# Performance work log

Hardware: AMD Instinct MI355X
Metric: run time of the kernel (lower is better)

The kernel has to match this reference:

```python
import jax, jax.numpy as jnp
import numpy as np

B, S, D, SIZE = 32, 2048, 1024, 1024

def setup_inputs() -> dict:
    key = jax.random.key(0)
    k1, k2, k3, k4, k5 = jax.random.split(key, 5)
    return {
        "inputs": jax.random.normal(k1, (B, S, D), dtype=jnp.float32),
        "g": jax.random.normal(k2, (B, D), dtype=jnp.float32),
        "WO": jax.random.normal(k3, (SIZE, D), dtype=jnp.float32) * 0.05,
        "WG": jax.random.normal(k4, (SIZE, D), dtype=jnp.float32) * 0.05,
        "v": jax.random.normal(k5, (1, SIZE), dtype=jnp.float32) * 0.05,
    }

def reference(inputs, g, WO, WG, v):
    # term1[b,s,k] = WO @ inputs[b,s]; term2[b,k] = WG @ g[b]
    term1 = jnp.einsum('kd,bsd->bsk', WO, inputs)
    term2 = jnp.einsum('kd,bd->bk', WG, g)
    tan_sum = jnp.tanh(term1 + term2[:, None, :])  # [B,S,SIZE]
    # final[b,s] = v @ tan_sum[b,s]  (v is [1,SIZE]); squeeze -> [B,S]
    return jnp.einsum('k,bsk->bs', v[0], tan_sum)
```

## Files before the change

### kernel.cpp

```cpp
#include <hip/hip_runtime.h>
#include <hip/hip_bf16.h>

#define BB   32
#define SS   2048
#define DD   1024
#define SZ   1024
#define MM   (BB*SS)

typedef short bf16x8 __attribute__((ext_vector_type(8)));
typedef float f32x4  __attribute__((ext_vector_type(4)));

__device__ __forceinline__ unsigned short f2bf(float x) {
    unsigned u = __float_as_uint(x);
    u += 0x7fffu + ((u >> 16) & 1u);
    return (unsigned short)(u >> 16);
}
__device__ __forceinline__ unsigned pack2_bf16(float a, float b) {
    return (unsigned)f2bf(a) | ((unsigned)f2bf(b) << 16);
}

__device__ __forceinline__ float ftanh(float x) {
    float e = __expf(2.0f * x);
    return 1.0f - 2.0f / (e + 1.0f);
}

__global__ void prep_kernel(const float* __restrict__ WO,
                            const float* __restrict__ WG,
                            const float* __restrict__ g,
                            unsigned short* __restrict__ WOb,
                            float* __restrict__ term2) {
    int bid = blockIdx.x, tid = threadIdx.x;
    if (bid < 1024) {
        int q = bid;
        int d = tid * 4;
        float4 w = *(const float4*)(WO + (size_t)q * DD + d);
        unsigned p0 = pack2_bf16(w.x, w.y), p1 = pack2_bf16(w.z, w.w);
        int dst = ((d >> 5) * 4096 + ((d >> 3) & 3) * 1024 + q) * 8 + (d & 7);
        *(uint2*)&WOb[dst] = make_uint2(p0, p1);
    } else {
        int id    = bid - 1024;
        int b     = id >> 4;
        int wave  = tid >> 6, lane = tid & 63;
        int kbase = (id & 15) * 64 + wave * 16;
        const float* gr = g + (size_t)b * DD + lane * 16;
        float4 g0 = *(const float4*)(gr + 0);
        float4 g1 = *(const float4*)(gr + 4);
        float4 g2 = *(const float4*)(gr + 8);
        float4 g3 = *(const float4*)(gr + 12);
        #pragma unroll
        for (int i = 0; i < 16; i++) {
            int k = kbase + i;
            const float* wr = WG + (size_t)k * DD + lane * 16;
            float4 a0 = *(const float4*)(wr + 0);
            float4 a1 = *(const float4*)(wr + 4);
            float4 a2 = *(const float4*)(wr + 8);
            float4 a3 = *(const float4*)(wr + 12);
            float s = a0.x*g0.x + a0.y*g0.y + a0.z*g0.z + a0.w*g0.w
                    + a1.x*g1.x + a1.y*g1.y + a1.z*g1.z + a1.w*g1.w
                    + a2.x*g2.x + a2.y*g2.y + a2.z*g2.z + a2.w*g2.w
                    + a3.x*g3.x + a3.y*g3.y + a3.z*g3.z + a3.w*g3.w;
            #pragma unroll
            for (int m = 1; m < 64; m <<= 1) s += __shfl_xor(s, m);
            if (lane == 0) term2[b * SZ + k] = s;
        }
    }
}

__global__ __launch_bounds__(256, 2) void fused_main(
    const float* __restrict__ Ain,
    const unsigned short* __restrict__ WOb,
    const float* __restrict__ term2,
    const float* __restrict__ v,
    float* __restrict__ out) {
    __shared__ unsigned short Abuf[2][4096];
    __shared__ unsigned short Bbuf[2][8192];
    __shared__ float part[2][128];

    const int tid  = threadIdx.x;
    const int wave = tid >> 6;
    const int lane = tid & 63;
    const int wm  = wave & 1, wn = wave >> 1;
    const int l15 = lane & 15;
    const int k8  = lane >> 4;

    const int bid     = blockIdx.x;
    const int logical = (bid & 7) * 256 + (bid >> 3);
    const int ntile = logical & 3;
    const int mtile = logical >> 2;
    const int m0 = mtile * 128;
    const int n0 = ntile * 256;
    const int bidx = m0 >> 11;

    f32x4 acc[4][8];
    #pragma unroll
    for (int i = 0; i < 4; i++)
        #pragma unroll
        for (int j = 0; j < 8; j++) acc[i][j] = (f32x4){0.f, 0.f, 0.f, 0.f};

    float4 areg[4];

    auto LOAD_A = [&](int k0) {
        #pragma unroll
        for (int r = 0; r < 4; r++) {
            int row = r * 32 + (tid >> 3);
            areg[r] = *(const float4*)(Ain + (size_t)(m0 + row) * DD + k0 + (tid & 7) * 4);
        }
    };
    auto WRITE_A = [&](int buf) {
        const int q = tid & 7, kg = q >> 1, half = q & 1;
        #pragma unroll
        for (int r = 0; r < 4; r++) {
            int row = r * 32 + (tid >> 3);
            unsigned p0 = pack2_bf16(areg[r].x, areg[r].y);
            unsigned p1 = pack2_bf16(areg[r].z, areg[r].w);
            *(uint2*)&Abuf[buf][(kg * 128 + row) * 8 + half * 4] = make_uint2(p0, p1);
        }
    };
    auto STAGE_B = [&](int buf, int kt) {
        #pragma unroll
        for (int r = 0; r < 4; r++) {
            const unsigned short* src = WOb + ((size_t)(kt * 4 + r) * 1024 + n0 + tid) * 8;
            __builtin_amdgcn_global_load_lds(
                (const __attribute__((address_space(1))) void*)src,
                (__attribute__((address_space(3))) void*)(&Bbuf[buf][(r * 256 + tid) * 8]),
                16, 0, 0);
        }
    };
    auto COMPUTE = [&](int buf) {
        bf16x8 afr[4], bfr[8];
        const int aoff = (k8 * 128 + wm * 64 + l15) * 8;
        const int boff = (k8 * 256 + wn * 128 + l15) * 8;
        #pragma unroll
        for (int mi = 0; mi < 4; mi++)
            afr[mi] = *(const bf16x8*)&Abuf[buf][aoff + mi * 128];
        #pragma unroll
        for (int ni = 0; ni < 8; ni++)
            bfr[ni] = *(const bf16x8*)&Bbuf[buf][boff + ni * 128];
        __builtin_amdgcn_s_setprio(1);
        #pragma unroll
        for (int ni = 0; ni < 8; ni++)
            #pragma unroll
            for (int mi = 0; mi < 4; mi++)
                acc[mi][ni] = __builtin_amdgcn_mfma_f32_16x16x32_bf16(
                    afr[mi], bfr[ni], acc[mi][ni], 0, 0, 0);
        __builtin_amdgcn_s_setprio(0);
    };

    LOAD_A(0);
    WRITE_A(0);
    __builtin_amdgcn_sched_barrier(0);
    STAGE_B(0, 0);
    __builtin_amdgcn_sched_barrier(0);
    LOAD_A(32);
    __builtin_amdgcn_sched_barrier(0);
    asm volatile("s_waitcnt vmcnt(4)" ::: "memory");
    asm volatile("s_waitcnt lgkmcnt(0)" ::: "memory");
    __builtin_amdgcn_sched_barrier(0);
    __builtin_amdgcn_s_barrier();

    for (int t = 0; t < 31; ++t) {
        const int buf = t & 1;
        WRITE_A(buf ^ 1);
        __builtin_amdgcn_sched_barrier(0);
        STAGE_B(buf ^ 1, t + 1);
        __builtin_amdgcn_sched_barrier(0);
        LOAD_A(((t + 2 <= 31) ? t + 2 : 31) << 5);
        __builtin_amdgcn_sched_barrier(0);
        COMPUTE(buf);
        __builtin_amdgcn_sched_barrier(0);
        asm volatile("s_waitcnt vmcnt(4)" ::: "memory");
        asm volatile("s_waitcnt lgkmcnt(0)" ::: "memory");
        __builtin_amdgcn_sched_barrier(0);
        __builtin_amdgcn_s_barrier();
    }
    COMPUTE(1);

    float rsum[4][4];
    #pragma unroll
    for (int mi = 0; mi < 4; mi++)
        #pragma unroll
        for (int r = 0; r < 4; r++) rsum[mi][r] = 0.f;

    #pragma unroll
    for (int ni = 0; ni < 8; ni++) {
        int gn = n0 + wn * 128 + ni * 16 + l15;
        float t2 = term2[bidx * SZ + gn];
        float vv = v[gn];
        #pragma unroll
        for (int mi = 0; mi < 4; mi++)
            #pragma unroll
            for (int r = 0; r < 4; r++)
                rsum[mi][r] += ftanh(acc[mi][ni][r] + t2) * vv;
    }
    #pragma unroll
    for (int mi = 0; mi < 4; mi++)
        #pragma unroll
        for (int r = 0; r < 4; r++) {
            float s = rsum[mi][r];
            s += __shfl_xor(s, 1, 16);
            s += __shfl_xor(s, 2, 16);
            s += __shfl_xor(s, 4, 16);
            s += __shfl_xor(s, 8, 16);
            rsum[mi][r] = s;
        }
    float val = 0.f;
    #pragma unroll
    for (int mi = 0; mi < 4; mi++)
        #pragma unroll
        for (int r = 0; r < 4; r++)
            if (l15 == mi * 4 + r) val = rsum[mi][r];
    {
        int mi = l15 >> 2, r = l15 & 3;
        part[wn][wm * 64 + mi * 16 + k8 * 4 + r] = val;
    }
    __syncthreads();
    if (tid < 128) atomicAdd(&out[m0 + tid], part[0][tid] + part[1][tid]);
}

extern "C" void kernel_launch(void* const* d_in, const int* in_sizes, int n_in,
                              void* d_out, int out_size, void* d_ws, size_t ws_size,
                              hipStream_t stream) {
    const float* inputs = (const float*)d_in[0];
    const float* g      = (const float*)d_in[1];
    const float* WO     = (const float*)d_in[2];
    const float* WG     = (const float*)d_in[3];
    const float* v      = (const float*)d_in[4];
    float* out = (float*)d_out;

    unsigned short* WOb = (unsigned short*)d_ws;
    float* term2 = (float*)((char*)d_ws + (size_t)SZ * DD * 2);

    (void)hipMemsetAsync(d_out, 0, sizeof(float) * MM, stream);
    prep_kernel<<<1024 + 512, 256, 0, stream>>>(WO, WG, g, WOb, term2);
    fused_main<<<(MM / 128) * (SZ / 256), 256, 0, stream>>>(inputs, WOb, term2, v, out);
}
```

Before: 534.1 us.

## Triple-buffer B tiles with two-ahead prefetch and use hardware bf16 pack

The weight tiles in LDS become triple-buffered, so the async global-to-LDS load for tile t+2 is issued before computing tile t, and the vmcnt wait is relaxed to cover the deeper pipeline. The A conversion and LDS write move after the MFMA block so the global load latency overlaps compute. The software float-to-bf16 rounding is replaced with the v_cvt_pk_bf16_f32 instruction. The extra LDS buffer raises shared memory per block, which may reduce occupancy at two blocks per CU.

```diff
diff --git a/kernel.cpp b/kernel.cpp
--- a/kernel.cpp
+++ b/kernel.cpp
@@ -17,6 +17,11 @@
 }
 __device__ __forceinline__ unsigned pack2_bf16(float a, float b) {
     return (unsigned)f2bf(a) | ((unsigned)f2bf(b) << 16);
+}
+__device__ __forceinline__ unsigned cvtpk_bf16(float lo, float hi) {
+    unsigned r;
+    asm("v_cvt_pk_bf16_f32 %0, %1, %2" : "=v"(r) : "v"(lo), "v"(hi));
+    return r;
 }
 
 __device__ __forceinline__ float ftanh(float x) {
@@ -73,7 +78,7 @@
     const float* __restrict__ v,
     float* __restrict__ out) {
     __shared__ unsigned short Abuf[2][4096];
-    __shared__ unsigned short Bbuf[2][8192];
+    __shared__ unsigned short Bbuf[3][8192];
     __shared__ float part[2][128];
 
     const int tid  = threadIdx.x;
@@ -111,8 +116,8 @@
         #pragma unroll
         for (int r = 0; r < 4; r++) {
             int row = r * 32 + (tid >> 3);
-            unsigned p0 = pack2_bf16(areg[r].x, areg[r].y);
-            unsigned p1 = pack2_bf16(areg[r].z, areg[r].w);
+            unsigned p0 = cvtpk_bf16(areg[r].x, areg[r].y);
+            unsigned p1 = cvtpk_bf16(areg[r].z, areg[r].w);
             *(uint2*)&Abuf[buf][(kg * 128 + row) * 8 + half * 4] = make_uint2(p0, p1);
         }
     };
@@ -126,16 +131,16 @@
                 16, 0, 0);
         }
     };
-    auto COMPUTE = [&](int buf) {
+    auto COMPUTE = [&](int abuf, int bbuf) {
         bf16x8 afr[4], bfr[8];
         const int aoff = (k8 * 128 + wm * 64 + l15) * 8;
         const int boff = (k8 * 256 + wn * 128 + l15) * 8;
         #pragma unroll
         for (int mi = 0; mi < 4; mi++)
-            afr[mi] = *(const bf16x8*)&Abuf[buf][aoff + mi * 128];
+            afr[mi] = *(const bf16x8*)&Abuf[abuf][aoff + mi * 128];
         #pragma unroll
         for (int ni = 0; ni < 8; ni++)
-            bfr[ni] = *(const bf16x8*)&Bbuf[buf][boff + ni * 128];
+            bfr[ni] = *(const bf16x8*)&Bbuf[bbuf][boff + ni * 128];
         __builtin_amdgcn_s_setprio(1);
         #pragma unroll
         for (int ni = 0; ni < 8; ni++)
@@ -147,33 +152,40 @@
     };
 
     LOAD_A(0);
+    __builtin_amdgcn_sched_barrier(0);
+    STAGE_B(0, 0);
+    __builtin_amdgcn_sched_barrier(0);
     WRITE_A(0);
     __builtin_amdgcn_sched_barrier(0);
-    STAGE_B(0, 0);
+    STAGE_B(1, 1);
     __builtin_amdgcn_sched_barrier(0);
     LOAD_A(32);
     __builtin_amdgcn_sched_barrier(0);
-    asm volatile("s_waitcnt vmcnt(4)" ::: "memory");
+    asm volatile("s_waitcnt vmcnt(8)" ::: "memory");
     asm volatile("s_waitcnt lgkmcnt(0)" ::: "memory");
     __builtin_amdgcn_sched_barrier(0);
     __builtin_amdgcn_s_barrier();
 
+    int bc = 0;
     for (int t = 0; t < 31; ++t) {
-        const int buf = t & 1;
-        WRITE_A(buf ^ 1);
-        __builtin_amdgcn_sched_barrier(0);
-        STAGE_B(buf ^ 1, t + 1);
-        __builtin_amdgcn_sched_barrier(0);
-        LOAD_A(((t + 2 <= 31) ? t + 2 : 31) << 5);
-        __builtin_amdgcn_sched_barrier(0);
-        COMPUTE(buf);
-        __builtin_amdgcn_sched_barrier(0);
-        asm volatile("s_waitcnt vmcnt(4)" ::: "memory");
+        const int ab = t & 1;
+        const int bs = (bc + 2 >= 3) ? bc - 1 : bc + 2;
+        const int tn = (t + 2 <= 31) ? t + 2 : 31;
+        STAGE_B(bs, tn);
+        __builtin_amdgcn_sched_barrier(0);
+        COMPUTE(ab, bc);
+        __builtin_amdgcn_sched_barrier(0);
+        WRITE_A(ab ^ 1);
+        __builtin_amdgcn_sched_barrier(0);
+        LOAD_A(tn << 5);
+        __builtin_amdgcn_sched_barrier(0);
+        asm volatile("s_waitcnt vmcnt(8)" ::: "memory");
         asm volatile("s_waitcnt lgkmcnt(0)" ::: "memory");
         __builtin_amdgcn_sched_barrier(0);
         __builtin_amdgcn_s_barrier();
-    }
-    COMPUTE(1);
+        bc = (bc + 1 >= 3) ? 0 : bc + 1;
+    }
+    COMPUTE(1, bc);
 
     float rsum[4][4];
     #pragma unroll
```

After: 518.3 us. 2.9% less time.
